# Optimization experiments

Measured on AMD Instinct MI355X. Metric: run time of the kernel, lower is better.

The kernel has to match this reference:

```python
import jax, jax.numpy as jnp
import numpy as np

B, F, E, K, O = 4096, 64, 16, 8, 32
NFEAT, HID = 100000, 1024
EPS = 1e-5
N_ITER = 50  # entmax bisection iterations (entmax package default)


def entmax15(x):
    # alpha=1.5 entmax via bisection, faithful to EntmaxBisectFunction.forward
    d = x.shape[-1]
    xs = x * 0.5  # X * (alpha - 1)
    mx = jnp.max(xs, axis=-1, keepdims=True)
    tau_lo = mx - 1.0                      # gp(1, 1.5) = 1
    tau_hi = mx - (1.0 / d) ** 0.5         # gp(1/d, 1.5)
    f_lo = jnp.sum(jnp.square(jnp.maximum(xs - tau_lo, 0.0)), -1, keepdims=True) - 1.0
    dm = tau_hi - tau_lo

    def body(i, carry):
        tau_lo, dm, _ = carry
        dm = dm * 0.5
        tau_m = tau_lo + dm
        f_m = jnp.sum(jnp.square(jnp.maximum(xs - tau_m, 0.0)), -1, keepdims=True) - 1.0
        tau_lo = jnp.where(f_m * f_lo >= 0, tau_m, tau_lo)
        return (tau_lo, dm, tau_m)

    _, _, tau_m = jax.lax.fori_loop(0, N_ITER, body, (tau_lo, dm, tau_lo))
    p = jnp.square(jnp.maximum(xs - tau_m, 0.0))
    return p / jnp.sum(p, -1, keepdims=True)


def bn_channels(x, g, b):
    # BatchNorm1d on (B, C, L): normalize over batch and L per channel C (train mode)
    m = jnp.mean(x, (0, 2), keepdims=True)
    v = jnp.var(x, (0, 2), keepdims=True)
    return (x - m) / jnp.sqrt(v + EPS) * g[None, :, None] + b[None, :, None]


def bn_feat(x, g, b):
    # BatchNorm1d on (B, C) (train mode, biased variance)
    m = jnp.mean(x, 0)
    v = jnp.var(x, 0)
    return (x - m) / jnp.sqrt(v + EPS) * g + b


def setup_inputs() -> dict:
    key = jax.random.key(0)
    ks = jax.random.split(key, 12)
    gain = 1.414
    aQ = gain * np.sqrt(6.0 / (O + E))
    aB = gain * np.sqrt(6.0 / (E + E))
    aV = gain * np.sqrt(6.0 / (O + F))
    D0 = K * O * E
    return {
        'x_id': jax.random.randint(ks[0], (B, F), 0, NFEAT),
        'x_value': jax.random.uniform(ks[1], (B, F), dtype=jnp.float32),
        'emb': jax.random.normal(ks[2], (NFEAT, E), dtype=jnp.float32) * 0.1,
        'emb_g': jnp.ones((F,), jnp.float32), 'emb_b': jnp.zeros((F,), jnp.float32),
        'Q': jax.random.uniform(ks[3], (K, O, E), jnp.float32, -aQ, aQ),
        'bil': jax.random.uniform(ks[4], (K, E, E), jnp.float32, -aB, aB),
        'vals': jax.random.uniform(ks[5], (K, O, F), jnp.float32, -aV, aV),
        'arm_g': jnp.ones((K * O,), jnp.float32), 'arm_b': jnp.zeros((K * O,), jnp.float32),
        'w1': jax.random.normal(ks[6], (HID, D0), jnp.float32) / np.sqrt(D0),
        'b1': jnp.zeros((HID,), jnp.float32),
        'g1': jnp.ones((HID,), jnp.float32), 'bt1': jnp.zeros((HID,), jnp.float32),
        'w2': jax.random.normal(ks[7], (HID, HID), jnp.float32) / np.sqrt(HID),
        'b2': jnp.zeros((HID,), jnp.float32),
        'g2': jnp.ones((HID,), jnp.float32), 'bt2': jnp.zeros((HID,), jnp.float32),
        'wout': jax.random.normal(ks[8], (1, HID), jnp.float32) / np.sqrt(HID),
        'bout': jnp.zeros((1,), jnp.float32),
    }


def reference(x_id, x_value, emb, emb_g, emb_b, Q, bil, vals, arm_g, arm_b,
              w1, b1, g1, bt1, w2, b2, g2, bt2, wout, bout):
    v = jnp.clip(x_value, 0.001, 1.0)
    xe = emb[x_id] * v[..., None]                       # B,F,E
    x_exp = bn_channels(jnp.exp(xe), emb_g, emb_b)       # B,F,E
    # bilinear attention scores + global context bias
    kq = jnp.einsum('kxy,koy->kox', bil, Q)              # K,O,E (fuse param contraction)
    sc = jnp.einsum('bfx,kox->bkof', xe, kq)             # B,K,O,F
    gc = jnp.einsum('bx,kox->bko', xe.sum(1), kq)        # B,K,O
    sg = entmax15(sc + gc[..., None])                    # B,K,O,F sparse gates
    aw = sg * vals[None]                                 # B,K,O,F
    arm = jnp.einsum('bfe,bkof->bkoe', x_exp, aw)        # B,K,O,E
    arm = arm.reshape(arm.shape[0], K * O, E)
    arm = bn_channels(arm, arm_g, arm_b).reshape(arm.shape[0], -1)
    h = jax.nn.relu(bn_feat(arm @ w1.T + b1, g1, bt1))
    h = jax.nn.relu(bn_feat(h @ w2.T + b2, g2, bt2))
    y = h @ wout.T + bout
    return y[:, 0]
```

## Files before the change

### kernel.cpp

```cpp
#include <hip/hip_runtime.h>

#define EPS 1e-5f

typedef __bf16 bf16;
typedef bf16 bf16x8 __attribute__((ext_vector_type(8)));
typedef float f32x4 __attribute__((ext_vector_type(4)));
typedef float f32x2 __attribute__((ext_vector_type(2)));

__device__ __forceinline__ void lds_cp16(void* lds, const void* g) {
  __builtin_amdgcn_global_load_lds(
      (const __attribute__((address_space(1))) void*)g,
      (__attribute__((address_space(3))) void*)lds, 16, 0, 0);
}

__device__ __forceinline__ f32x4 mfma_bf16(bf16x8 a, bf16x8 b, f32x4 c) {
  return __builtin_amdgcn_mfma_f32_16x16x32_bf16(a, b, c, 0, 0, 0);
}

__global__ void k_zero(float* p) { p[blockIdx.x * 256 + threadIdx.x] = 0.0f; }

__global__ void k_embed(const int* __restrict__ x_id, const float* __restrict__ x_val,
                        const float* __restrict__ emb, float* __restrict__ xe) {
  int g = blockIdx.x * 256 + threadIdx.x;
  int id = x_id[g];
  float v = fminf(fmaxf(x_val[g], 0.001f), 1.0f);
  const float4* er = (const float4*)(emb + (size_t)id * 16);
  float4* xo = (float4*)(xe + (size_t)g * 16);
#pragma unroll
  for (int j = 0; j < 4; ++j) {
    float4 e = er[j];
    e.x *= v; e.y *= v; e.z *= v; e.w *= v;
    xo[j] = e;
  }
}

__global__ void k_expstats(const float* __restrict__ xe, float* __restrict__ es,
                           float* __restrict__ eq) {
  int t = threadIdx.x;
  int b0 = blockIdx.x * 16;
  float4 s4 = {0, 0, 0, 0}, q4 = {0, 0, 0, 0};
  for (int i = 0; i < 16; ++i) {
    float4 v = ((const float4*)(xe + (size_t)(b0 + i) * 1024))[t];
    float4 e;
    e.x = __expf(v.x); e.y = __expf(v.y); e.z = __expf(v.z); e.w = __expf(v.w);
    s4.x += e.x; s4.y += e.y; s4.z += e.z; s4.w += e.w;
    q4.x += e.x * e.x; q4.y += e.y * e.y; q4.z += e.z * e.z; q4.w += e.w * e.w;
  }
  float s = (s4.x + s4.y) + (s4.z + s4.w);
  float q = (q4.x + q4.y) + (q4.z + q4.w);
  s += __shfl_xor(s, 1, 64); s += __shfl_xor(s, 2, 64);
  q += __shfl_xor(q, 1, 64); q += __shfl_xor(q, 2, 64);
  if ((t & 3) == 0) {
    int f = t >> 2;
    atomicAdd(es + f, s);
    atomicAdd(eq + f, q);
  }
}

__global__ void k_expfin(const float* __restrict__ es, const float* __restrict__ eq,
                         const float* __restrict__ g_, const float* __restrict__ b_,
                         float* __restrict__ oa, float* __restrict__ ob) {
  int f = threadIdx.x;
  float mean = es[f] * (1.0f / 65536.0f);
  float var = eq[f] * (1.0f / 65536.0f) - mean * mean;
  float a = g_[f] * rsqrtf(var + EPS);
  oa[f] = a;
  ob[f] = b_[f] - mean * a;
}

__global__ void k_kq(const float* __restrict__ Qw, const float* __restrict__ bil,
                     float* __restrict__ kq) {
  int t = threadIdx.x;
  int k = t >> 5;
  float qv[16];
#pragma unroll
  for (int y = 0; y < 16; ++y) qv[y] = Qw[t * 16 + y];
  const float* bl = bil + k * 256;
#pragma unroll
  for (int x = 0; x < 16; ++x) {
    float s = 0.f;
#pragma unroll
    for (int y = 0; y < 16; ++y) s += bl[x * 16 + y] * qv[y];
    kq[t * 16 + x] = 0.5f * s;
  }
}

__global__ __launch_bounds__(256, 2) void k_attn(
    const float* __restrict__ xe_g, const float* __restrict__ kq_g,
    const float* __restrict__ eba, const float* __restrict__ ebb,
    const float* __restrict__ vals, bf16* __restrict__ arm) {
  __shared__ __align__(16) float s_xe[64 * 16];
  __shared__ float s_sum[16];
  __shared__ __align__(16) bf16 s_aw[256 * 72];
  __shared__ __align__(16) bf16 s_X[16 * 72];
  const int t = threadIdx.x;
  const int b = blockIdx.x;
  const f32x2 z2 = {0.f, 0.f};

  ((float4*)s_xe)[t] = ((const float4*)(xe_g + (size_t)b * 1024))[t];
  __syncthreads();

  if (t < 16) {
    float s = 0.f;
#pragma unroll
    for (int f = 0; f < 64; ++f) s += s_xe[f * 16 + t];
    s_sum[t] = s;
  }
  {
    int f = t >> 2, e0 = (t & 3) * 4;
    float a = eba[f], c = ebb[f];
#pragma unroll
    for (int j = 0; j < 4; ++j) {
      float v = __expf(s_xe[f * 16 + e0 + j]) * a + c;
      s_X[(e0 + j) * 72 + f] = (bf16)v;
    }
  }
  __syncthreads();

  f32x2 kq2[8];
  {
    const f32x4* g4 = (const f32x4*)(kq_g + t * 16);
#pragma unroll
    for (int j = 0; j < 4; ++j) {
      f32x4 v = g4[j];
      kq2[2 * j] = __builtin_shufflevector(v, v, 0, 1);
      kq2[2 * j + 1] = __builtin_shufflevector(v, v, 2, 3);
    }
  }
  float gc;
  {
    const f32x2* ss = (const f32x2*)s_sum;
    f32x2 g2 = z2;
#pragma unroll
    for (int i = 0; i < 8; ++i) g2 += ss[i] * kq2[i];
    gc = g2.x + g2.y;
  }

  f32x2 xs2[32];
#pragma unroll
  for (int f = 0; f < 64; ++f) {
    const f32x4* xr = (const f32x4*)(s_xe + f * 16);
    f32x4 A0 = xr[0], A1 = xr[1], A2 = xr[2], A3 = xr[3];
    f32x2 acc = z2;
    acc += __builtin_shufflevector(A0, A0, 0, 1) * kq2[0];
    acc += __builtin_shufflevector(A0, A0, 2, 3) * kq2[1];
    acc += __builtin_shufflevector(A1, A1, 0, 1) * kq2[2];
    acc += __builtin_shufflevector(A1, A1, 2, 3) * kq2[3];
    acc += __builtin_shufflevector(A2, A2, 0, 1) * kq2[4];
    acc += __builtin_shufflevector(A2, A2, 2, 3) * kq2[5];
    acc += __builtin_shufflevector(A3, A3, 0, 1) * kq2[6];
    acc += __builtin_shufflevector(A3, A3, 2, 3) * kq2[7];
    float v = (acc.x + acc.y) + gc;
    if (f & 1) xs2[f >> 1].y = v; else xs2[f >> 1].x = v;
  }

  f32x2 m2 = xs2[0];
#pragma unroll
  for (int i = 1; i < 32; ++i) m2 = __builtin_elementwise_max(m2, xs2[i]);
  float mx = fmaxf(m2.x, m2.y);

  float tau_lo = mx - 1.0f;
  float dm = 0.875f;
#pragma unroll
  for (int it = 0; it < 7; ++it) {
    dm *= 0.5f;
    float tm = tau_lo + dm;
    f32x2 t2 = {tm, tm};
    f32x2 c2 = z2;
#pragma unroll
    for (int i = 0; i < 32; ++i) {
      f32x2 d = xs2[i] - t2;
      d = __builtin_elementwise_max(d, z2);
      c2 += d * d;
    }
    tau_lo = ((c2.x + c2.y) - 1.0f >= 0.f) ? tm : tau_lo;
  }
  float tau = tau_lo + dm;
#pragma unroll
  for (int r = 0; r < 2; ++r) {
    f32x2 t2 = {tau, tau};
    f32x2 S2 = z2, Q2 = z2;
    float cnt = 0.f;
#pragma unroll
    for (int i = 0; i < 32; ++i) {
      f32x2 y = xs2[i] - t2;
      f32x2 m = __builtin_elementwise_max(y, z2);
      S2 += m; Q2 += m * m;
      cnt += (y.x > 0.f ? 1.f : 0.f) + (y.y > 0.f ? 1.f : 0.f);
    }
    float S1 = S2.x + S2.y, Q1 = Q2.x + Q2.y;
    float disc = fmaxf(S1 * S1 - cnt * (Q1 - 1.0f), 0.f);
    tau += (S1 - sqrtf(disc)) / cnt;
  }
  f32x2 Zv = z2;
  {
    f32x2 t2 = {tau, tau};
#pragma unroll
    for (int i = 0; i < 32; ++i) {
      f32x2 d = __builtin_elementwise_max(xs2[i] - t2, z2);
      f32x2 p = d * d;
      xs2[i] = p;
      Zv += p;
    }
  }
  float inv = 1.0f / (Zv.x + Zv.y);

  const float4* vg = (const float4*)(vals + t * 64);
#pragma unroll
  for (int f8 = 0; f8 < 64; f8 += 8) {
    float4 v0 = vg[f8 / 4], v1 = vg[f8 / 4 + 1];
    union { bf16 h[8]; uint4 u; } pk;
    pk.h[0] = (bf16)(xs2[f8 / 2].x * inv * v0.x);
    pk.h[1] = (bf16)(xs2[f8 / 2].y * inv * v0.y);
    pk.h[2] = (bf16)(xs2[f8 / 2 + 1].x * inv * v0.z);
    pk.h[3] = (bf16)(xs2[f8 / 2 + 1].y * inv * v0.w);
    pk.h[4] = (bf16)(xs2[f8 / 2 + 2].x * inv * v1.x);
    pk.h[5] = (bf16)(xs2[f8 / 2 + 2].y * inv * v1.y);
    pk.h[6] = (bf16)(xs2[f8 / 2 + 3].x * inv * v1.z);
    pk.h[7] = (bf16)(xs2[f8 / 2 + 3].y * inv * v1.w);
    *(uint4*)(s_aw + t * 72 + f8) = pk.u;
  }
  __syncthreads();

  const int w = t >> 6, lane = t & 63;
  f32x4 acc[4];
#pragma unroll
  for (int mt = 0; mt < 4; ++mt) acc[mt] = (f32x4){0.f, 0.f, 0.f, 0.f};
#pragma unroll
  for (int ks = 0; ks < 2; ++ks) {
    bf16x8 bfrag = *(const bf16x8*)(s_X + (lane & 15) * 72 + ks * 32 + (lane >> 4) * 8);
#pragma unroll
    for (int mt = 0; mt < 4; ++mt) {
      int row = (w * 4 + mt) * 16 + (lane & 15);
      bf16x8 afrag = *(const bf16x8*)(s_aw + row * 72 + ks * 32 + (lane >> 4) * 8);
      acc[mt] = mfma_bf16(afrag, bfrag, acc[mt]);
    }
  }
  bf16* armb = arm + (size_t)b * 4096;
#pragma unroll
  for (int mt = 0; mt < 4; ++mt) {
    int ko0 = (w * 4 + mt) * 16 + (lane >> 4) * 4;
#pragma unroll
    for (int r = 0; r < 4; ++r)
      armb[(ko0 + r) * 16 + (lane & 15)] = (bf16)acc[mt][r];
  }
}

__global__ void k_armstats(const bf16* __restrict__ arm, float* __restrict__ as_,
                           float* __restrict__ aq) {
  int t = threadIdx.x;
  int b0 = blockIdx.x * 16;
  float s = 0.f, q = 0.f;
  for (int i = 0; i < 16; ++i) {
    const bf16* p = arm + (size_t)(b0 + i) * 4096 + t * 16;
    bf16x8 v0 = *(const bf16x8*)p;
    bf16x8 v1 = *(const bf16x8*)(p + 8);
#pragma unroll
    for (int j = 0; j < 8; ++j) {
      float a = (float)v0[j], c = (float)v1[j];
      s += a + c; q += a * a + c * c;
    }
  }
  atomicAdd(as_ + t, s);
  atomicAdd(aq + t, q);
}

__global__ void k_armfin(const float* __restrict__ as_, const float* __restrict__ aq,
                         const float* __restrict__ g_, const float* __restrict__ b_,
                         float* __restrict__ oa, float* __restrict__ oc) {
  int ko = threadIdx.x;
  float mean = as_[ko] * (1.0f / 65536.0f);
  float var = aq[ko] * (1.0f / 65536.0f) - mean * mean;
  float a = g_[ko] * rsqrtf(var + EPS);
  oa[ko] = a;
  oc[ko] = b_[ko] - mean * a;
}

__global__ void k_cvtw1s(const float* __restrict__ s, const float* __restrict__ a,
                         bf16* __restrict__ d, int n4) {
  int stride = gridDim.x * 256;
  for (int i = blockIdx.x * 256 + threadIdx.x; i < n4; i += stride) {
    float4 v = ((const float4*)s)[i];
    float av = a[(i >> 2) & 255];
    union { bf16 h[4]; uint2 u; } p;
    p.h[0] = (bf16)(v.x * av); p.h[1] = (bf16)(v.y * av);
    p.h[2] = (bf16)(v.z * av); p.h[3] = (bf16)(v.w * av);
    *(uint2*)(d + (size_t)i * 4) = p.u;
  }
}

__global__ void k_bias1(const float* __restrict__ w1, const float* __restrict__ c,
                        const float* __restrict__ b1, float* __restrict__ bias1) {
  int t = threadIdx.x;
  int w = t >> 6, lane = t & 63;
  int h = blockIdx.x * 4 + w;
  const float4* row = (const float4*)(w1 + (size_t)h * 4096);
  float s = 0.f;
#pragma unroll
  for (int it = 0; it < 16; ++it) {
    int j4 = it * 64 + lane;
    float4 v = row[j4];
    float cj = c[j4 >> 2];
    s += cj * ((v.x + v.y) + (v.z + v.w));
  }
#pragma unroll
  for (int off = 32; off > 0; off >>= 1) s += __shfl_xor(s, off, 64);
  if (lane == 0) bias1[h] = b1[h] + s;
}

__global__ void k_cvt(const float* __restrict__ s, bf16* __restrict__ d, int n4) {
  int stride = gridDim.x * 256;
  for (int i = blockIdx.x * 256 + threadIdx.x; i < n4; i += stride) {
    float4 v = ((const float4*)s)[i];
    union { bf16 h[4]; uint2 u; } p;
    p.h[0] = (bf16)v.x; p.h[1] = (bf16)v.y; p.h[2] = (bf16)v.z; p.h[3] = (bf16)v.w;
    *(uint2*)(d + (size_t)i * 4) = p.u;
  }
}

__global__ __launch_bounds__(256, 2) void gemm_bt(
    const bf16* __restrict__ A, const bf16* __restrict__ Bw,
    const float* __restrict__ bias, float* __restrict__ C,
    float* __restrict__ csum, float* __restrict__ csq, int Kd) {
  __shared__ __align__(16) bf16 sA[128 * 32];
  __shared__ __align__(16) bf16 sB[64 * 32];
  const int t = threadIdx.x;
  const int w = t >> 6, lane = t & 63;
  const int m0 = blockIdx.x * 128, n0 = blockIdx.y * 64;

  f32x4 acc[2][4];
#pragma unroll
  for (int i = 0; i < 2; ++i)
#pragma unroll
    for (int j = 0; j < 4; ++j) acc[i][j] = (f32x4){0.f, 0.f, 0.f, 0.f};

  for (int kt = 0; kt < Kd; kt += 32) {
#pragma unroll
    for (int c = 0; c < 2; ++c) {
      int idx = c * 256 + t;
      int row = idx >> 2, ch = idx & 3;
      int sch = ch ^ ((row >> 1) & 3);
      lds_cp16(sA + idx * 8, A + (size_t)(m0 + row) * Kd + kt + sch * 8);
    }
    {
      int row = t >> 2, ch = t & 3;
      int sch = ch ^ ((row >> 1) & 3);
      lds_cp16(sB + t * 8, Bw + (size_t)(n0 + row) * Kd + kt + sch * 8);
    }
    __syncthreads();
    bf16x8 af[2], bfr[4];
#pragma unroll
    for (int mt = 0; mt < 2; ++mt) {
      int row = w * 32 + mt * 16 + (lane & 15);
      int ch = (lane >> 4) ^ ((row >> 1) & 3);
      af[mt] = *(const bf16x8*)(sA + row * 32 + ch * 8);
    }
#pragma unroll
    for (int nt = 0; nt < 4; ++nt) {
      int row = nt * 16 + (lane & 15);
      int ch = (lane >> 4) ^ ((row >> 1) & 3);
      bfr[nt] = *(const bf16x8*)(sB + row * 32 + ch * 8);
    }
#pragma unroll
    for (int mt = 0; mt < 2; ++mt)
#pragma unroll
      for (int nt = 0; nt < 4; ++nt)
        acc[mt][nt] = mfma_bf16(af[mt], bfr[nt], acc[mt][nt]);
    __syncthreads();
  }

#pragma unroll
  for (int nt = 0; nt < 4; ++nt) {
    int ncol = n0 + nt * 16 + (lane & 15);
    float bv = bias[ncol];
    float s = 0.f, q = 0.f;
#pragma unroll
    for (int mt = 0; mt < 2; ++mt) {
      int mr = m0 + w * 32 + mt * 16 + (lane >> 4) * 4;
#pragma unroll
      for (int r = 0; r < 4; ++r) {
        float v = acc[mt][nt][r] + bv;
        C[(size_t)(mr + r) * 1024 + ncol] = v;
        s += v; q += v * v;
      }
    }
    s += __shfl_xor(s, 16, 64); s += __shfl_xor(s, 32, 64);
    q += __shfl_xor(q, 16, 64); q += __shfl_xor(q, 32, 64);
    if ((lane >> 4) == 0) {
      atomicAdd(csum + ncol, s);
      atomicAdd(csq + ncol, q);
    }
  }
}

__global__ void k_colfin(const float* __restrict__ s, const float* __restrict__ q,
                         const float* __restrict__ g_, const float* __restrict__ bt,
                         float* __restrict__ a, float* __restrict__ c) {
  int h = blockIdx.x * 256 + threadIdx.x;
  float mean = s[h] * (1.0f / 4096.0f);
  float var = q[h] * (1.0f / 4096.0f) - mean * mean;
  float av = g_[h] * rsqrtf(var + EPS);
  a[h] = av;
  c[h] = bt[h] - mean * av;
}

__global__ void k_h1bf(const float* __restrict__ C1, const float* __restrict__ a,
                       const float* __restrict__ c, bf16* __restrict__ H1) {
  int i4 = blockIdx.x * 256 + threadIdx.x;
  int col0 = (i4 * 4) & 1023;
  float4 v = ((const float4*)C1)[i4];
  float4 av = *(const float4*)(a + col0);
  float4 cv = *(const float4*)(c + col0);
  union { bf16 h[4]; uint2 u; } pk;
  pk.h[0] = (bf16)fmaxf(v.x * av.x + cv.x, 0.f);
  pk.h[1] = (bf16)fmaxf(v.y * av.y + cv.y, 0.f);
  pk.h[2] = (bf16)fmaxf(v.z * av.z + cv.z, 0.f);
  pk.h[3] = (bf16)fmaxf(v.w * av.w + cv.w, 0.f);
  *(uint2*)(H1 + (size_t)i4 * 4) = pk.u;
}

__global__ __launch_bounds__(256) void k_out(const float* __restrict__ C2,
                                             const float* __restrict__ a,
                                             const float* __restrict__ c,
                                             const float* __restrict__ wout,
                                             const float* __restrict__ bout,
                                             float* __restrict__ y) {
  int t = threadIdx.x;
  int w = t >> 6, lane = t & 63;
  int row = blockIdx.x * 4 + w;
  const float* cr = C2 + (size_t)row * 1024;
  float s = 0.f;
#pragma unroll
  for (int j = 0; j < 16; ++j) {
    int col = j * 64 + lane;
    float v = fmaxf(cr[col] * a[col] + c[col], 0.f);
    s += v * wout[col];
  }
#pragma unroll
  for (int off = 32; off > 0; off >>= 1) s += __shfl_xor(s, off, 64);
  if (lane == 0) y[row] = s + bout[0];
}

extern "C" void kernel_launch(void* const* d_in, const int* in_sizes, int n_in,
                              void* d_out, int out_size, void* d_ws, size_t ws_size,
                              hipStream_t stream) {
  (void)in_sizes; (void)n_in; (void)out_size; (void)ws_size;
  const int* x_id = (const int*)d_in[0];
  const float* x_value = (const float*)d_in[1];
  const float* emb = (const float*)d_in[2];
  const float* emb_g = (const float*)d_in[3];
  const float* embb = (const float*)d_in[4];
  const float* Qw = (const float*)d_in[5];
  const float* bil = (const float*)d_in[6];
  const float* vals = (const float*)d_in[7];
  const float* arm_g = (const float*)d_in[8];
  const float* arm_b = (const float*)d_in[9];
  const float* w1 = (const float*)d_in[10];
  const float* b1 = (const float*)d_in[11];
  const float* g1 = (const float*)d_in[12];
  const float* bt1 = (const float*)d_in[13];
  const float* w2 = (const float*)d_in[14];
  const float* b2 = (const float*)d_in[15];
  const float* g2 = (const float*)d_in[16];
  const float* bt2 = (const float*)d_in[17];
  const float* wout = (const float*)d_in[18];
  const float* bout = (const float*)d_in[19];

  char* w = (char*)d_ws;
  float* ws_xe = (float*)w;
  float* ws_C = ws_xe;
  bf16* ws_arm = (bf16*)(w + 16777216);
  bf16* ws_H1 = (bf16*)(w + 50331648);
  bf16* ws_w1b = (bf16*)(w + 58720256);
  bf16* ws_w2b = (bf16*)(w + 67108864);
  float* ws_kq = (float*)(w + 69206016);
  float* st = (float*)(w + 69222400);
  float* es = st;
  float* eq = es + 64;
  float* as_ = eq + 64;
  float* aq = as_ + 256;
  float* s1 = aq + 256;
  float* q1 = s1 + 1024;
  float* s2 = q1 + 1024;
  float* q2 = s2 + 1024;
  float* eb_a = st + 5120;
  float* eb_b = eb_a + 64;
  float* arm_a = eb_b + 64;
  float* arm_c = arm_a + 256;
  float* a1c = arm_c + 256;
  float* c1c = a1c + 1024;
  float* a2c = c1c + 1024;
  float* c2c = a2c + 1024;
  float* bias1 = c2c + 1024;

  k_zero<<<20, 256, 0, stream>>>(st);
  k_embed<<<1024, 256, 0, stream>>>(x_id, x_value, emb, ws_xe);
  k_expstats<<<256, 256, 0, stream>>>(ws_xe, es, eq);
  k_expfin<<<1, 64, 0, stream>>>(es, eq, emb_g, embb, eb_a, eb_b);
  k_kq<<<1, 256, 0, stream>>>(Qw, bil, ws_kq);
  k_attn<<<4096, 256, 0, stream>>>(ws_xe, ws_kq, eb_a, eb_b, vals, ws_arm);
  k_armstats<<<256, 256, 0, stream>>>(ws_arm, as_, aq);
  k_armfin<<<1, 256, 0, stream>>>(as_, aq, arm_g, arm_b, arm_a, arm_c);
  k_cvtw1s<<<1024, 256, 0, stream>>>(w1, arm_a, ws_w1b, 1048576);
  k_bias1<<<256, 256, 0, stream>>>(w1, arm_c, b1, bias1);
  k_cvt<<<256, 256, 0, stream>>>(w2, ws_w2b, 262144);
  gemm_bt<<<dim3(32, 16), 256, 0, stream>>>(ws_arm, ws_w1b, bias1, ws_C, s1, q1, 4096);
  k_colfin<<<4, 256, 0, stream>>>(s1, q1, g1, bt1, a1c, c1c);
  k_h1bf<<<4096, 256, 0, stream>>>(ws_C, a1c, c1c, ws_H1);
  gemm_bt<<<dim3(32, 16), 256, 0, stream>>>(ws_H1, ws_w2b, b2, ws_C, s2, q2, 1024);
  k_colfin<<<4, 256, 0, stream>>>(s2, q2, g2, bt2, a2c, c2c);
  k_out<<<1024, 256, 0, stream>>>(ws_C, a2c, c2c, wout, bout, (float*)d_out);
}
```

Before: 358.1 us.

## Fuse stats kernels, drop BN-cancelled biases, raise attn occupancy via LDS aliasing

Fuses embedding with exp-BN statistics and weight conversions into fewer kernels. Replaces atomic accumulation with per-block partial sums reduced in the finalize steps. Drops biases (b1, b2, arm_b shift) that cancel under train-mode batchnorm. Aliases LDS buffers in the attention kernel so it can target four blocks per CU, and stages its output through LDS for coalesced stores. The higher occupancy target risks register spills in the entmax loop.

```diff
diff --git a/kernel.cpp b/kernel.cpp
--- a/kernel.cpp
+++ b/kernel.cpp
@@ -17,59 +17,44 @@
   return __builtin_amdgcn_mfma_f32_16x16x32_bf16(a, b, c, 0, 0, 0);
 }
 
-__global__ void k_zero(float* p) { p[blockIdx.x * 256 + threadIdx.x] = 0.0f; }
-
 __global__ void k_embed(const int* __restrict__ x_id, const float* __restrict__ x_val,
-                        const float* __restrict__ emb, float* __restrict__ xe) {
-  int g = blockIdx.x * 256 + threadIdx.x;
-  int id = x_id[g];
-  float v = fminf(fmaxf(x_val[g], 0.001f), 1.0f);
-  const float4* er = (const float4*)(emb + (size_t)id * 16);
-  float4* xo = (float4*)(xe + (size_t)g * 16);
-#pragma unroll
-  for (int j = 0; j < 4; ++j) {
-    float4 e = er[j];
-    e.x *= v; e.y *= v; e.z *= v; e.w *= v;
-    xo[j] = e;
-  }
-}
-
-__global__ void k_expstats(const float* __restrict__ xe, float* __restrict__ es,
-                           float* __restrict__ eq) {
-  int t = threadIdx.x;
-  int b0 = blockIdx.x * 16;
-  float4 s4 = {0, 0, 0, 0}, q4 = {0, 0, 0, 0};
-  for (int i = 0; i < 16; ++i) {
-    float4 v = ((const float4*)(xe + (size_t)(b0 + i) * 1024))[t];
-    float4 e;
-    e.x = __expf(v.x); e.y = __expf(v.y); e.z = __expf(v.z); e.w = __expf(v.w);
-    s4.x += e.x; s4.y += e.y; s4.z += e.z; s4.w += e.w;
-    q4.x += e.x * e.x; q4.y += e.y * e.y; q4.z += e.z * e.z; q4.w += e.w * e.w;
-  }
-  float s = (s4.x + s4.y) + (s4.z + s4.w);
-  float q = (q4.x + q4.y) + (q4.z + q4.w);
-  s += __shfl_xor(s, 1, 64); s += __shfl_xor(s, 2, 64);
-  q += __shfl_xor(q, 1, 64); q += __shfl_xor(q, 2, 64);
-  if ((t & 3) == 0) {
-    int f = t >> 2;
-    atomicAdd(es + f, s);
-    atomicAdd(eq + f, q);
-  }
-}
-
-__global__ void k_expfin(const float* __restrict__ es, const float* __restrict__ eq,
-                         const float* __restrict__ g_, const float* __restrict__ b_,
-                         float* __restrict__ oa, float* __restrict__ ob) {
-  int f = threadIdx.x;
-  float mean = es[f] * (1.0f / 65536.0f);
-  float var = eq[f] * (1.0f / 65536.0f) - mean * mean;
-  float a = g_[f] * rsqrtf(var + EPS);
-  oa[f] = a;
-  ob[f] = b_[f] - mean * a;
-}
-
-__global__ void k_kq(const float* __restrict__ Qw, const float* __restrict__ bil,
-                     float* __restrict__ kq) {
+                        const float* __restrict__ emb, float* __restrict__ xe,
+                        float* __restrict__ es_p, float* __restrict__ eq_p) {
+  int t = threadIdx.x, bid = blockIdx.x;
+  float s = 0.f, q = 0.f;
+#pragma unroll
+  for (int it = 0; it < 4; ++it) {
+    int g = it * 65536 + bid * 256 + t;
+    int id = x_id[g];
+    float v = fminf(fmaxf(x_val[g], 0.001f), 1.0f);
+    const float4* er = (const float4*)(emb + (size_t)id * 16);
+    float4* xo = (float4*)(xe + (size_t)g * 16);
+#pragma unroll
+    for (int j = 0; j < 4; ++j) {
+      float4 e = er[j];
+      e.x *= v; e.y *= v; e.z *= v; e.w *= v;
+      xo[j] = e;
+      float a0 = __expf(e.x), a1 = __expf(e.y), a2 = __expf(e.z), a3 = __expf(e.w);
+      s += (a0 + a1) + (a2 + a3);
+      q += (a0 * a0 + a1 * a1) + (a2 * a2 + a3 * a3);
+    }
+  }
+  __shared__ float rs[256], rq[256];
+  rs[t] = s; rq[t] = q;
+  __syncthreads();
+  if (t < 64) {
+    float S = rs[t] + rs[t + 64] + rs[t + 128] + rs[t + 192];
+    float Q = rq[t] + rq[t + 64] + rq[t + 128] + rq[t + 192];
+    es_p[bid * 64 + t] = S;
+    eq_p[bid * 64 + t] = Q;
+  }
+}
+
+__global__ void k_prep(const float* __restrict__ Qw, const float* __restrict__ bil,
+                       float* __restrict__ kq, const float* __restrict__ es_p,
+                       const float* __restrict__ eq_p, const float* __restrict__ g_,
+                       const float* __restrict__ b_, float* __restrict__ oa,
+                       float* __restrict__ ob) {
   int t = threadIdx.x;
   int k = t >> 5;
   float qv[16];
@@ -83,16 +68,27 @@
     for (int y = 0; y < 16; ++y) s += bl[x * 16 + y] * qv[y];
     kq[t * 16 + x] = 0.5f * s;
   }
-}
-
-__global__ __launch_bounds__(256, 2) void k_attn(
+  if (t < 64) {
+    float S = 0.f, Q = 0.f;
+    for (int i = 0; i < 256; ++i) { S += es_p[i * 64 + t]; Q += eq_p[i * 64 + t]; }
+    float mean = S * (1.0f / 65536.0f);
+    float var = Q * (1.0f / 65536.0f) - mean * mean;
+    float a = g_[t] * rsqrtf(var + EPS);
+    oa[t] = a;
+    ob[t] = b_[t] - mean * a;
+  }
+}
+
+__global__ __launch_bounds__(256, 4) void k_attn(
     const float* __restrict__ xe_g, const float* __restrict__ kq_g,
     const float* __restrict__ eba, const float* __restrict__ ebb,
     const float* __restrict__ vals, bf16* __restrict__ arm) {
-  __shared__ __align__(16) float s_xe[64 * 16];
-  __shared__ float s_sum[16];
-  __shared__ __align__(16) bf16 s_aw[256 * 72];
-  __shared__ __align__(16) bf16 s_X[16 * 72];
+  __shared__ __align__(16) unsigned char smem[39168];
+  float* s_xe = (float*)smem;
+  float* s_sum = (float*)(smem + 4096);
+  bf16* s_aw = (bf16*)smem;
+  float* s_out = (float*)smem;
+  bf16* s_X = (bf16*)(smem + 36864);
   const int t = threadIdx.x;
   const int b = blockIdx.x;
   const f32x2 z2 = {0.f, 0.f};
@@ -153,6 +149,7 @@
     float v = (acc.x + acc.y) + gc;
     if (f & 1) xs2[f >> 1].y = v; else xs2[f >> 1].x = v;
   }
+  __syncthreads();
 
   f32x2 m2 = xs2[0];
 #pragma unroll
@@ -236,22 +233,29 @@
       acc[mt] = mfma_bf16(afrag, bfrag, acc[mt]);
     }
   }
-  bf16* armb = arm + (size_t)b * 4096;
+  __syncthreads();
 #pragma unroll
   for (int mt = 0; mt < 4; ++mt) {
     int ko0 = (w * 4 + mt) * 16 + (lane >> 4) * 4;
 #pragma unroll
     for (int r = 0; r < 4; ++r)
-      armb[(ko0 + r) * 16 + (lane & 15)] = (bf16)acc[mt][r];
-  }
-}
-
-__global__ void k_armstats(const bf16* __restrict__ arm, float* __restrict__ as_,
-                           float* __restrict__ aq) {
+      s_out[(lane & 15) * 257 + ko0 + r] = acc[mt][r];
+  }
+  __syncthreads();
+  union { bf16 h[16]; uint4 u[2]; } pk;
+#pragma unroll
+  for (int e = 0; e < 16; ++e) pk.h[e] = (bf16)s_out[e * 257 + t];
+  uint4* dst = (uint4*)(arm + (size_t)b * 4096 + t * 16);
+  dst[0] = pk.u[0];
+  dst[1] = pk.u[1];
+}
+
+__global__ void k_armstats(const bf16* __restrict__ arm, float* __restrict__ as_p,
+                           float* __restrict__ aq_p) {
   int t = threadIdx.x;
-  int b0 = blockIdx.x * 16;
+  int b0 = blockIdx.x * 64;
   float s = 0.f, q = 0.f;
-  for (int i = 0; i < 16; ++i) {
+  for (int i = 0; i < 64; ++i) {
     const bf16* p = arm + (size_t)(b0 + i) * 4096 + t * 16;
     bf16x8 v0 = *(const bf16x8*)p;
     bf16x8 v1 = *(const bf16x8*)(p + 8);
@@ -261,69 +265,51 @@
       s += a + c; q += a * a + c * c;
     }
   }
-  atomicAdd(as_ + t, s);
-  atomicAdd(aq + t, q);
-}
-
-__global__ void k_armfin(const float* __restrict__ as_, const float* __restrict__ aq,
-                         const float* __restrict__ g_, const float* __restrict__ b_,
-                         float* __restrict__ oa, float* __restrict__ oc) {
-  int ko = threadIdx.x;
-  float mean = as_[ko] * (1.0f / 65536.0f);
-  float var = aq[ko] * (1.0f / 65536.0f) - mean * mean;
-  float a = g_[ko] * rsqrtf(var + EPS);
-  oa[ko] = a;
-  oc[ko] = b_[ko] - mean * a;
-}
-
-__global__ void k_cvtw1s(const float* __restrict__ s, const float* __restrict__ a,
-                         bf16* __restrict__ d, int n4) {
-  int stride = gridDim.x * 256;
-  for (int i = blockIdx.x * 256 + threadIdx.x; i < n4; i += stride) {
-    float4 v = ((const float4*)s)[i];
-    float av = a[(i >> 2) & 255];
-    union { bf16 h[4]; uint2 u; } p;
-    p.h[0] = (bf16)(v.x * av); p.h[1] = (bf16)(v.y * av);
-    p.h[2] = (bf16)(v.z * av); p.h[3] = (bf16)(v.w * av);
-    *(uint2*)(d + (size_t)i * 4) = p.u;
-  }
-}
-
-__global__ void k_bias1(const float* __restrict__ w1, const float* __restrict__ c,
-                        const float* __restrict__ b1, float* __restrict__ bias1) {
-  int t = threadIdx.x;
-  int w = t >> 6, lane = t & 63;
-  int h = blockIdx.x * 4 + w;
-  const float4* row = (const float4*)(w1 + (size_t)h * 4096);
-  float s = 0.f;
-#pragma unroll
-  for (int it = 0; it < 16; ++it) {
-    int j4 = it * 64 + lane;
-    float4 v = row[j4];
-    float cj = c[j4 >> 2];
-    s += cj * ((v.x + v.y) + (v.z + v.w));
-  }
-#pragma unroll
-  for (int off = 32; off > 0; off >>= 1) s += __shfl_xor(s, off, 64);
-  if (lane == 0) bias1[h] = b1[h] + s;
-}
-
-__global__ void k_cvt(const float* __restrict__ s, bf16* __restrict__ d, int n4) {
-  int stride = gridDim.x * 256;
-  for (int i = blockIdx.x * 256 + threadIdx.x; i < n4; i += stride) {
-    float4 v = ((const float4*)s)[i];
-    union { bf16 h[4]; uint2 u; } p;
-    p.h[0] = (bf16)v.x; p.h[1] = (bf16)v.y; p.h[2] = (bf16)v.z; p.h[3] = (bf16)v.w;
-    *(uint2*)(d + (size_t)i * 4) = p.u;
+  as_p[blockIdx.x * 256 + t] = s;
+  aq_p[blockIdx.x * 256 + t] = q;
+}
+
+__global__ void k_cvtw(const float* __restrict__ w1, const float* __restrict__ w2,
+                       const float* __restrict__ as_p, const float* __restrict__ aq_p,
+                       const float* __restrict__ arm_g, bf16* __restrict__ d1,
+                       bf16* __restrict__ d2) {
+  int t = threadIdx.x, bid = blockIdx.x;
+  if (bid < 256) {
+    __shared__ float scale[256];
+    float s = 0.f, q = 0.f;
+    for (int i = 0; i < 64; ++i) { s += as_p[i * 256 + t]; q += aq_p[i * 256 + t]; }
+    float mean = s * (1.0f / 65536.0f);
+    float var = q * (1.0f / 65536.0f) - mean * mean;
+    scale[t] = arm_g[t] * rsqrtf(var + EPS);
+    __syncthreads();
+#pragma unroll
+    for (int it = 0; it < 16; ++it) {
+      int i = it * 65536 + bid * 256 + t;
+      float4 v = ((const float4*)w1)[i];
+      float av = scale[(i >> 2) & 255];
+      union { bf16 h[4]; uint2 u; } p;
+      p.h[0] = (bf16)(v.x * av); p.h[1] = (bf16)(v.y * av);
+      p.h[2] = (bf16)(v.z * av); p.h[3] = (bf16)(v.w * av);
+      *(uint2*)(d1 + (size_t)i * 4) = p.u;
+    }
+  } else {
+#pragma unroll
+    for (int it = 0; it < 16; ++it) {
+      int i = it * 16384 + (bid - 256) * 256 + t;
+      float4 v = ((const float4*)w2)[i];
+      union { bf16 h[4]; uint2 u; } p;
+      p.h[0] = (bf16)v.x; p.h[1] = (bf16)v.y; p.h[2] = (bf16)v.z; p.h[3] = (bf16)v.w;
+      *(uint2*)(d2 + (size_t)i * 4) = p.u;
+    }
   }
 }
 
 __global__ __launch_bounds__(256, 2) void gemm_bt(
-    const bf16* __restrict__ A, const bf16* __restrict__ Bw,
-    const float* __restrict__ bias, float* __restrict__ C,
-    float* __restrict__ csum, float* __restrict__ csq, int Kd) {
+    const bf16* __restrict__ A, const bf16* __restrict__ Bw, float* __restrict__ C,
+    float* __restrict__ sp, float* __restrict__ sq, int Kd) {
   __shared__ __align__(16) bf16 sA[128 * 32];
   __shared__ __align__(16) bf16 sB[64 * 32];
+  __shared__ float sredS[4][64], sredQ[4][64];
   const int t = threadIdx.x;
   const int w = t >> 6, lane = t & 63;
   const int m0 = blockIdx.x * 128, n0 = blockIdx.y * 64;
@@ -372,33 +358,38 @@
 #pragma unroll
   for (int nt = 0; nt < 4; ++nt) {
     int ncol = n0 + nt * 16 + (lane & 15);
-    float bv = bias[ncol];
     float s = 0.f, q = 0.f;
 #pragma unroll
     for (int mt = 0; mt < 2; ++mt) {
       int mr = m0 + w * 32 + mt * 16 + (lane >> 4) * 4;
 #pragma unroll
       for (int r = 0; r < 4; ++r) {
-        float v = acc[mt][nt][r] + bv;
+        float v = acc[mt][nt][r];
         C[(size_t)(mr + r) * 1024 + ncol] = v;
         s += v; q += v * v;
       }
     }
     s += __shfl_xor(s, 16, 64); s += __shfl_xor(s, 32, 64);
     q += __shfl_xor(q, 16, 64); q += __shfl_xor(q, 32, 64);
-    if ((lane >> 4) == 0) {
-      atomicAdd(csum + ncol, s);
-      atomicAdd(csq + ncol, q);
-    }
-  }
-}
-
-__global__ void k_colfin(const float* __restrict__ s, const float* __restrict__ q,
+    if (lane < 16) { sredS[w][nt * 16 + lane] = s; sredQ[w][nt * 16 + lane] = q; }
+  }
+  __syncthreads();
+  if (t < 64) {
+    float S = sredS[0][t] + sredS[1][t] + sredS[2][t] + sredS[3][t];
+    float Q = sredQ[0][t] + sredQ[1][t] + sredQ[2][t] + sredQ[3][t];
+    sp[blockIdx.x * 1024 + n0 + t] = S;
+    sq[blockIdx.x * 1024 + n0 + t] = Q;
+  }
+}
+
+__global__ void k_colfin(const float* __restrict__ sp, const float* __restrict__ sq,
                          const float* __restrict__ g_, const float* __restrict__ bt,
                          float* __restrict__ a, float* __restrict__ c) {
   int h = blockIdx.x * 256 + threadIdx.x;
-  float mean = s[h] * (1.0f / 4096.0f);
-  float var = q[h] * (1.0f / 4096.0f) - mean * mean;
+  float S = 0.f, Q = 0.f;
+  for (int i = 0; i < 32; ++i) { S += sp[i * 1024 + h]; Q += sq[i * 1024 + h]; }
+  float mean = S * (1.0f / 4096.0f);
+  float var = Q * (1.0f / 4096.0f) - mean * mean;
   float av = g_[h] * rsqrtf(var + EPS);
   a[h] = av;
   c[h] = bt[h] - mean * av;
@@ -454,60 +445,47 @@
   const float* bil = (const float*)d_in[6];
   const float* vals = (const float*)d_in[7];
   const float* arm_g = (const float*)d_in[8];
-  const float* arm_b = (const float*)d_in[9];
   const float* w1 = (const float*)d_in[10];
-  const float* b1 = (const float*)d_in[11];
   const float* g1 = (const float*)d_in[12];
   const float* bt1 = (const float*)d_in[13];
   const float* w2 = (const float*)d_in[14];
-  const float* b2 = (const float*)d_in[15];
   const float* g2 = (const float*)d_in[16];
   const float* bt2 = (const float*)d_in[17];
   const float* wout = (const float*)d_in[18];
   const float* bout = (const float*)d_in[19];
 
   char* w = (char*)d_ws;
-  float* ws_xe = (float*)w;
-  float* ws_C = ws_xe;
+  float* ws_A = (float*)w;
   bf16* ws_arm = (bf16*)(w + 16777216);
-  bf16* ws_H1 = (bf16*)(w + 50331648);
-  bf16* ws_w1b = (bf16*)(w + 58720256);
-  bf16* ws_w2b = (bf16*)(w + 67108864);
-  float* ws_kq = (float*)(w + 69206016);
-  float* st = (float*)(w + 69222400);
-  float* es = st;
-  float* eq = es + 64;
-  float* as_ = eq + 64;
-  float* aq = as_ + 256;
-  float* s1 = aq + 256;
-  float* q1 = s1 + 1024;
-  float* s2 = q1 + 1024;
-  float* q2 = s2 + 1024;
-  float* eb_a = st + 5120;
+  bf16* ws_w1b = (bf16*)(w + 50331648);
+  bf16* ws_H1 = ws_w1b;
+  bf16* ws_w2b = (bf16*)(w + 58720256);
+  float* ws_kq = (float*)(w + 60817408);
+  float* misc = (float*)(w + 60833792);
+  float* es_p = misc;
+  float* eq_p = es_p + 16384;
+  float* as_p = eq_p + 16384;
+  float* aq_p = as_p + 16384;
+  float* sp1 = aq_p + 16384;
+  float* sq1 = sp1 + 32768;
+  float* sp2 = sq1 + 32768;
+  float* sq2 = sp2 + 32768;
+  float* eb_a = sq2 + 32768;
   float* eb_b = eb_a + 64;
-  float* arm_a = eb_b + 64;
-  float* arm_c = arm_a + 256;
-  float* a1c = arm_c + 256;
+  float* a1c = eb_b + 64;
   float* c1c = a1c + 1024;
   float* a2c = c1c + 1024;
   float* c2c = a2c + 1024;
-  float* bias1 = c2c + 1024;
-
-  k_zero<<<20, 256, 0, stream>>>(st);
-  k_embed<<<1024, 256, 0, stream>>>(x_id, x_value, emb, ws_xe);
-  k_expstats<<<256, 256, 0, stream>>>(ws_xe, es, eq);
-  k_expfin<<<1, 64, 0, stream>>>(es, eq, emb_g, embb, eb_a, eb_b);
-  k_kq<<<1, 256, 0, stream>>>(Qw, bil, ws_kq);
-  k_attn<<<4096, 256, 0, stream>>>(ws_xe, ws_kq, eb_a, eb_b, vals, ws_arm);
-  k_armstats<<<256, 256, 0, stream>>>(ws_arm, as_, aq);
-  k_armfin<<<1, 256, 0, stream>>>(as_, aq, arm_g, arm_b, arm_a, arm_c);
-  k_cvtw1s<<<1024, 256, 0, stream>>>(w1, arm_a, ws_w1b, 1048576);
-  k_bias1<<<256, 256, 0, stream>>>(w1, arm_c, b1, bias1);
-  k_cvt<<<256, 256, 0, stream>>>(w2, ws_w2b, 262144);
-  gemm_bt<<<dim3(32, 16), 256, 0, stream>>>(ws_arm, ws_w1b, bias1, ws_C, s1, q1, 4096);
-  k_colfin<<<4, 256, 0, stream>>>(s1, q1, g1, bt1, a1c, c1c);
-  k_h1bf<<<4096, 256, 0, stream>>>(ws_C, a1c, c1c, ws_H1);
-  gemm_bt<<<dim3(32, 16), 256, 0, stream>>>(ws_H1, ws_w2b, b2, ws_C, s2, q2, 1024);
-  k_colfin<<<4, 256, 0, stream>>>(s2, q2, g2, bt2, a2c, c2c);
-  k_out<<<1024, 256, 0, stream>>>(ws_C, a2c, c2c, wout, bout, (float*)d_out);
-}
+
+  k_embed<<<256, 256, 0, stream>>>(x_id, x_value, emb, ws_A, es_p, eq_p);
+  k_prep<<<1, 256, 0, stream>>>(Qw, bil, ws_kq, es_p, eq_p, emb_g, embb, eb_a, eb_b);
+  k_attn<<<4096, 256, 0, stream>>>(ws_A, ws_kq, eb_a, eb_b, vals, ws_arm);
+  k_armstats<<<64, 256, 0, stream>>>(ws_arm, as_p, aq_p);
+  k_cvtw<<<320, 256, 0, stream>>>(w1, w2, as_p, aq_p, arm_g, ws_w1b, ws_w2b);
+  gemm_bt<<<dim3(32, 16), 256, 0, stream>>>(ws_arm, ws_w1b, ws_A, sp1, sq1, 4096);
+  k_colfin<<<4, 256, 0, stream>>>(sp1, sq1, g1, bt1, a1c, c1c);
+  k_h1bf<<<4096, 256, 0, stream>>>(ws_A, a1c, c1c, ws_H1);
+  gemm_bt<<<dim3(32, 16), 256, 0, stream>>>(ws_H1, ws_w2b, ws_A, sp2, sq2, 1024);
+  k_colfin<<<4, 256, 0, stream>>>(sp2, sq2, g2, bt2, a2c, c2c);
+  k_out<<<1024, 256, 0, stream>>>(ws_A, a2c, c2c, wout, bout, (float*)d_out);
+}
```

After: 341.8 us. 4.6% less time.
